# Performance work log

Hardware: AMD Instinct MI355X
Metric: run time of the kernel (lower is better)

## Reference

```python
import jax, jax.numpy as jnp
import numpy as np

WS = 8  # window size
NUM_HEAD = 8
DIM_HEAD = 64


def _rel_pos_index(ws):
    coords = np.stack(np.meshgrid(np.arange(ws), np.arange(ws), indexing='ij'))  # (2, ws, ws)
    cf = coords.reshape(2, -1)                       # (2, A)
    rel = cf[:, :, None] - cf[:, None, :]            # (2, A, A)
    rel = rel.transpose(1, 2, 0).astype(np.int32)    # (A, A, 2)
    rel[:, :, 0] += ws - 1
    rel[:, :, 1] += ws - 1
    rel[:, :, 0] *= 2 * ws - 1
    return jnp.asarray(rel.sum(-1))                  # (A, A) int32


def setup_inputs() -> dict:
    key = jax.random.key(0)
    k0, k1, k2 = jax.random.split(key, 3)
    B, Hh, dh, H, W = 4, NUM_HEAD, DIM_HEAD, 128, 128
    C = Hh * dh
    qkv = jax.random.normal(k0, (B, Hh, 3 * dh, H, W), dtype=jnp.float32)
    logit_scale = jnp.log(10.0) * jnp.ones((Hh, 1, 1), dtype=jnp.float32)
    rpb_table = 0.02 * jax.random.normal(k1, ((2 * WS - 1) * (2 * WS - 1), Hh), dtype=jnp.float32)
    proj_w = 0.02 * jax.random.normal(k2, (C, C), dtype=jnp.float32)
    proj_b = jnp.zeros((C,), dtype=jnp.float32)
    rel_index = _rel_pos_index(WS)
    return {"qkv": qkv, "logit_scale": logit_scale, "rpb_table": rpb_table,
            "proj_w": proj_w, "proj_b": proj_b, "rel_index": rel_index}


def reference(qkv, logit_scale, rpb_table, proj_w, proj_b, rel_index):
    B, Hh, C3, H, W = qkv.shape
    ws = WS
    dh = C3 // 3
    A = ws * ws
    nH, nW = H // ws, W // ws
    # window partition: (B, Hh, C3, H, W) -> (B*nH*nW, Hh, A, C3)
    x = qkv.reshape(B, Hh, C3, nH, ws, nW, ws)
    x = x.transpose(0, 3, 5, 1, 4, 6, 2).reshape(-1, Hh, A, C3)
    q, k, v = jnp.split(x, 3, axis=-1)
    # cosine attention: L2-normalize q, k (eps matches F.normalize)
    q = q / jnp.maximum(jnp.linalg.norm(q, axis=-1, keepdims=True), 1e-12)
    k = k / jnp.maximum(jnp.linalg.norm(k, axis=-1, keepdims=True), 1e-12)
    attn = jnp.einsum('whqd,whkd->whqk', q, k)
    scale = jnp.exp(jnp.minimum(logit_scale, jnp.log(100.0)))  # clamp max=log(1/0.01)
    attn = attn * scale[None]
    # relative position bias: (A,A,Hh) -> (1,Hh,A,A)
    bias = rpb_table[rel_index.reshape(-1)].reshape(A, A, Hh).transpose(2, 0, 1)
    attn = jax.nn.softmax(attn + bias[None], axis=-1)
    out = jnp.einsum('whqk,whkd->whqd', attn, v)  # (B*nH*nW, Hh, A, dh)
    # window unpartition -> (B, Hh*dh, H, W)
    out = out.reshape(B, nH, nW, Hh, ws, ws, dh)
    out = out.transpose(0, 3, 6, 1, 4, 2, 5).reshape(B, Hh * dh, H, W)
    # 1x1 conv projection
    out = jnp.einsum('oc,bchw->bohw', proj_w, out) + proj_b[None, :, None, None]
    return out
```

## Files before the change

### kernel.cpp

```cpp
#include <hip/hip_runtime.h>

typedef _Float16 f16;
typedef f16 f16x2 __attribute__((ext_vector_type(2)));
typedef f16 f16x4 __attribute__((ext_vector_type(4)));
typedef f16 f16x8 __attribute__((ext_vector_type(8)));
typedef float floatx4 __attribute__((ext_vector_type(4)));

#define LDS_AS(p) ((__attribute__((address_space(3))) unsigned int*)(p))
#define GLB_AS(p) ((const __attribute__((address_space(1))) unsigned int*)(p))

__device__ __forceinline__ void gload16(const void* g, void* l) {
  __builtin_amdgcn_global_load_lds(GLB_AS(g), LDS_AS(l), 16, 0, 0);
}

__global__ __launch_bounds__(256) void wconv_kernel(const float* __restrict__ w,
                                                    f16* __restrict__ wh) {
  const int i = (blockIdx.x * 256 + threadIdx.x) * 4;
  const float4 v = *(const float4*)(w + i);
  f16x4 o;
  o.x = (f16)v.x; o.y = (f16)v.y; o.z = (f16)v.z; o.w = (f16)v.w;
  *(f16x4*)(wh + i) = o;
}

__global__ __launch_bounds__(256) void attn_kernel(
    const float* __restrict__ qkv, const float* __restrict__ logit_scale,
    const float* __restrict__ rpb, const int* __restrict__ rel_index,
    f16* __restrict__ X) {
  __shared__ f16 qs[64 * 72];
  __shared__ f16 ks[64 * 72];
  __shared__ f16 vs[64 * 72];
  __shared__ f16 ps[64 * 72];
  __shared__ float partial[4][64];

  const int bid = blockIdx.x;
  const int h   = bid & 7;
  const int win = bid >> 3;
  const int wx  = win & 15;
  const int wy  = (win >> 4) & 15;
  const int b   = win >> 8;

  const int tid  = threadIdx.x;
  const int wave = tid >> 6;
  const int lane = tid & 63;

  {
    const int a  = lane;
    const int ty = a >> 3, tx = a & 7;
    const int poff = (wy * 8 + ty) * 128 + wx * 8 + tx;
    const size_t headbase = (size_t)((b * 8 + h) * 192) * 16384 + poff;
    const int cbase = (wave & 1) * 32;
    const int qk = (wave < 2) ? 0 : 64;
    const float* src = qkv + headbase + (size_t)(qk + cbase) * 16384;
    float vals[32];
    float ssq = 0.f;
#pragma unroll
    for (int i = 0; i < 32; i++) {
      float v = src[(size_t)i * 16384];
      vals[i] = v;
      ssq += v * v;
    }
    partial[wave][a] = ssq;

    const float* vsrc = qkv + headbase + (size_t)(128 + wave * 16) * 16384;
    float vv[16];
#pragma unroll
    for (int i = 0; i < 16; i++) vv[i] = vsrc[(size_t)i * 16384];

    __syncthreads();
    const float tot = partial[wave & 2][a] + partial[(wave & 2) | 1][a];
    const float rs = 1.0f / fmaxf(sqrtf(tot), 1e-12f);
    f16* dst = ((wave < 2) ? qs : ks) + a * 72 + cbase;
#pragma unroll
    for (int i = 0; i < 16; i++) {
      f16x2 pr;
      pr.x = (f16)(vals[2 * i] * rs);
      pr.y = (f16)(vals[2 * i + 1] * rs);
      *(f16x2*)(dst + 2 * i) = pr;
    }
#pragma unroll
    for (int i = 0; i < 16; i++) vs[(wave * 16 + i) * 72 + a] = (f16)vv[i];
  }
  __syncthreads();

  const int fr = lane & 15;
  const int g  = lane >> 4;
  const int m0 = wave * 16;
  const float scale = __expf(fminf(logit_scale[h], 4.60517019f));

  floatx4 acc[4];
  {
    const f16x8 a0 = *(const f16x8*)(qs + (m0 + fr) * 72 + g * 8);
    const f16x8 a1 = *(const f16x8*)(qs + (m0 + fr) * 72 + 32 + g * 8);
#pragma unroll
    for (int nt = 0; nt < 4; nt++) {
      const f16x8 b0 = *(const f16x8*)(ks + (nt * 16 + fr) * 72 + g * 8);
      const f16x8 b1 = *(const f16x8*)(ks + (nt * 16 + fr) * 72 + 32 + g * 8);
      floatx4 z = {0.f, 0.f, 0.f, 0.f};
      z = __builtin_amdgcn_mfma_f32_16x16x32_f16(a0, b0, z, 0, 0, 0);
      z = __builtin_amdgcn_mfma_f32_16x16x32_f16(a1, b1, z, 0, 0, 0);
      acc[nt] = z;
    }
  }

#pragma unroll
  for (int r = 0; r < 4; r++) {
    const int m = m0 + g * 4 + r;
    float v0[4];
    float mx = -1e30f;
#pragma unroll
    for (int nt = 0; nt < 4; nt++) {
      const int n = nt * 16 + fr;
      const float val = acc[nt][r] * scale + rpb[rel_index[m * 64 + n] * 8 + h];
      v0[nt] = val;
      mx = fmaxf(mx, val);
    }
    mx = fmaxf(mx, __shfl_xor(mx, 1));
    mx = fmaxf(mx, __shfl_xor(mx, 2));
    mx = fmaxf(mx, __shfl_xor(mx, 4));
    mx = fmaxf(mx, __shfl_xor(mx, 8));
    float s = 0.f;
#pragma unroll
    for (int nt = 0; nt < 4; nt++) {
      v0[nt] = __expf(v0[nt] - mx);
      s += v0[nt];
    }
    s += __shfl_xor(s, 1);
    s += __shfl_xor(s, 2);
    s += __shfl_xor(s, 4);
    s += __shfl_xor(s, 8);
    const float rinv = 1.0f / s;
#pragma unroll
    for (int nt = 0; nt < 4; nt++)
      ps[m * 72 + nt * 16 + fr] = (f16)(v0[nt] * rinv);
  }

  floatx4 oacc[4];
  {
    const f16x8 pa0 = *(const f16x8*)(ps + (m0 + fr) * 72 + g * 8);
    const f16x8 pa1 = *(const f16x8*)(ps + (m0 + fr) * 72 + 32 + g * 8);
#pragma unroll
    for (int dt = 0; dt < 4; dt++) {
      const f16x8 vb0 = *(const f16x8*)(vs + (dt * 16 + fr) * 72 + g * 8);
      const f16x8 vb1 = *(const f16x8*)(vs + (dt * 16 + fr) * 72 + 32 + g * 8);
      floatx4 z = {0.f, 0.f, 0.f, 0.f};
      z = __builtin_amdgcn_mfma_f32_16x16x32_f16(pa0, vb0, z, 0, 0, 0);
      z = __builtin_amdgcn_mfma_f32_16x16x32_f16(pa1, vb1, z, 0, 0, 0);
      oacc[dt] = z;
    }
  }

#pragma unroll
  for (int r = 0; r < 4; r++) {
    const int m = m0 + g * 4 + r;
    const int ty = m >> 3, tx = m & 7;
    const size_t npix = (size_t)(b * 128 + wy * 8 + ty) * 128 + wx * 8 + tx;
    f16* xp = X + npix * 512 + h * 64;
#pragma unroll
    for (int dt = 0; dt < 4; dt++) xp[dt * 16 + fr] = (f16)oacc[dt][r];
  }
}

__global__ __launch_bounds__(256) void proj_kernel(
    const f16* __restrict__ Wh, const f16* __restrict__ X,
    const float* __restrict__ bias, float* __restrict__ out) {
  __shared__ f16 As[128 * 32];
  __shared__ f16 Bs[128 * 32];

  const int tid  = threadIdx.x;
  const int lane = tid & 63;
  const int wave = tid >> 6;
  const int o0 = (blockIdx.x & 3) * 128;
  const int p0 = (blockIdx.x >> 2) * 128;

  const int fr = lane & 15, g = lane >> 4;
  const int wr = wave >> 1, wc = wave & 1;

  floatx4 acc[4][4] = {};

  const int r0 = tid >> 2;
  const int c0 = (tid & 3) * 8;
  const f16* gA0 = Wh + (size_t)(o0 + r0) * 512 + c0;
  const f16* gA1 = Wh + (size_t)(o0 + 64 + r0) * 512 + c0;
  const f16* gB0 = X + (size_t)(p0 + r0) * 512 + c0;
  const f16* gB1 = X + (size_t)(p0 + 64 + r0) * 512 + c0;
  f16* lA0 = As + tid * 8;
  f16* lA1 = As + (256 + tid) * 8;
  f16* lB0 = Bs + tid * 8;
  f16* lB1 = Bs + (256 + tid) * 8;

  for (int kc = 0; kc < 512; kc += 32) {
    gload16(gA0 + kc, lA0);
    gload16(gA1 + kc, lA1);
    gload16(gB0 + kc, lB0);
    gload16(gB1 + kc, lB1);
    __syncthreads();
    f16x8 af[4], bfr[4];
#pragma unroll
    for (int mt = 0; mt < 4; mt++)
      af[mt] = *(const f16x8*)(As + (wr * 64 + mt * 16 + fr) * 32 + g * 8);
#pragma unroll
    for (int nt = 0; nt < 4; nt++)
      bfr[nt] = *(const f16x8*)(Bs + (wc * 64 + nt * 16 + fr) * 32 + g * 8);
#pragma unroll
    for (int mt = 0; mt < 4; mt++)
#pragma unroll
      for (int nt = 0; nt < 4; nt++)
        acc[mt][nt] = __builtin_amdgcn_mfma_f32_16x16x32_f16(af[mt], bfr[nt],
                                                             acc[mt][nt], 0, 0, 0);
    __syncthreads();
  }

  const int bidx = p0 >> 14;
  const int rem0 = p0 & 16383;
#pragma unroll
  for (int mt = 0; mt < 4; mt++) {
#pragma unroll
    for (int r = 0; r < 4; r++) {
      const int o = o0 + wr * 64 + mt * 16 + g * 4 + r;
      const float bv = bias[o];
      float* op = out + ((size_t)(bidx * 512 + o) << 14) + rem0 + wc * 64;
#pragma unroll
      for (int nt = 0; nt < 4; nt++) op[nt * 16 + fr] = acc[mt][nt][r] + bv;
    }
  }
}

extern "C" void kernel_launch(void* const* d_in, const int* in_sizes, int n_in,
                              void* d_out, int out_size, void* d_ws, size_t ws_size,
                              hipStream_t stream) {
  const float* qkv         = (const float*)d_in[0];
  const float* logit_scale = (const float*)d_in[1];
  const float* rpb         = (const float*)d_in[2];
  const float* proj_w      = (const float*)d_in[3];
  const float* proj_b      = (const float*)d_in[4];
  const int*   rel_index   = (const int*)d_in[5];
  float* out = (float*)d_out;

  f16* Wh = (f16*)d_ws;
  f16* X  = (f16*)((char*)d_ws + (512 * 512 * 2));

  hipLaunchKernelGGL(wconv_kernel, dim3(256), dim3(256), 0, stream, proj_w, Wh);
  hipLaunchKernelGGL(attn_kernel, dim3(8192), dim3(256), 0, stream,
                     qkv, logit_scale, rpb, rel_index, X);
  hipLaunchKernelGGL(proj_kernel, dim3(2048), dim3(256), 0, stream,
                     Wh, X, proj_b, out);
}
```

Before: 653.3 us.

## Vectorize attention qkv loads and widen swizzled projection K tile

```diff
diff --git a/kernel.cpp b/kernel.cpp
--- a/kernel.cpp
+++ b/kernel.cpp
@@ -30,7 +30,6 @@
   __shared__ f16 ks[64 * 72];
   __shared__ f16 vs[64 * 72];
   __shared__ f16 ps[64 * 72];
-  __shared__ float partial[4][64];
 
   const int bid = blockIdx.x;
   const int h   = bid & 7;
@@ -44,41 +43,61 @@
   const int lane = tid & 63;
 
   {
-    const int a  = lane;
-    const int ty = a >> 3, tx = a & 7;
-    const int poff = (wy * 8 + ty) * 128 + wx * 8 + tx;
-    const size_t headbase = (size_t)((b * 8 + h) * 192) * 16384 + poff;
-    const int cbase = (wave & 1) * 32;
-    const int qk = (wave < 2) ? 0 : 64;
-    const float* src = qkv + headbase + (size_t)(qk + cbase) * 16384;
-    float vals[32];
+    const int c    = tid >> 2;
+    const int quad = tid & 3;
+    const int xh   = quad & 1;
+    const int tyb  = quad >> 1;
+    const size_t base = (size_t)((b * 8 + h) * 192) * 16384 +
+                        (size_t)(wy * 8) * 128 + wx * 8 + xh * 4;
+    const float* qp = qkv + base + (size_t)c * 16384;
+    const float* kp = qkv + base + (size_t)(64 + c) * 16384;
+    const float* vp = qkv + base + (size_t)(128 + c) * 16384;
+#pragma unroll
+    for (int j = 0; j < 4; j++) {
+      const int ty = 2 * j + tyb;
+      const int t0 = ty * 8 + xh * 4;
+      const float4 qv = *(const float4*)(qp + ty * 128);
+      const float4 kv = *(const float4*)(kp + ty * 128);
+      const float4 vv = *(const float4*)(vp + ty * 128);
+      qs[(t0 + 0) * 72 + c] = (f16)qv.x;
+      qs[(t0 + 1) * 72 + c] = (f16)qv.y;
+      qs[(t0 + 2) * 72 + c] = (f16)qv.z;
+      qs[(t0 + 3) * 72 + c] = (f16)qv.w;
+      ks[(t0 + 0) * 72 + c] = (f16)kv.x;
+      ks[(t0 + 1) * 72 + c] = (f16)kv.y;
+      ks[(t0 + 2) * 72 + c] = (f16)kv.z;
+      ks[(t0 + 3) * 72 + c] = (f16)kv.w;
+      vs[c * 72 + t0 + 0] = (f16)vv.x;
+      vs[c * 72 + t0 + 1] = (f16)vv.y;
+      vs[c * 72 + t0 + 2] = (f16)vv.z;
+      vs[c * 72 + t0 + 3] = (f16)vv.w;
+    }
+  }
+  __syncthreads();
+
+  {
+    const int token = (tid & 127) >> 1;
+    const int half  = tid & 1;
+    f16* rowp = ((tid < 128) ? qs : ks) + token * 72 + half * 32;
+    f16x8 d[4];
     float ssq = 0.f;
 #pragma unroll
-    for (int i = 0; i < 32; i++) {
-      float v = src[(size_t)i * 16384];
-      vals[i] = v;
-      ssq += v * v;
-    }
-    partial[wave][a] = ssq;
-
-    const float* vsrc = qkv + headbase + (size_t)(128 + wave * 16) * 16384;
-    float vv[16];
-#pragma unroll
-    for (int i = 0; i < 16; i++) vv[i] = vsrc[(size_t)i * 16384];
-
-    __syncthreads();
-    const float tot = partial[wave & 2][a] + partial[(wave & 2) | 1][a];
-    const float rs = 1.0f / fmaxf(sqrtf(tot), 1e-12f);
-    f16* dst = ((wave < 2) ? qs : ks) + a * 72 + cbase;
-#pragma unroll
-    for (int i = 0; i < 16; i++) {
-      f16x2 pr;
-      pr.x = (f16)(vals[2 * i] * rs);
-      pr.y = (f16)(vals[2 * i + 1] * rs);
-      *(f16x2*)(dst + 2 * i) = pr;
-    }
-#pragma unroll
-    for (int i = 0; i < 16; i++) vs[(wave * 16 + i) * 72 + a] = (f16)vv[i];
+    for (int i = 0; i < 4; i++) {
+      d[i] = *(const f16x8*)(rowp + i * 8);
+#pragma unroll
+      for (int e = 0; e < 8; e++) {
+        const float f = (float)d[i][e];
+        ssq += f * f;
+      }
+    }
+    ssq += __shfl_xor(ssq, 1);
+    const float rs = 1.0f / fmaxf(sqrtf(ssq), 1e-12f);
+#pragma unroll
+    for (int i = 0; i < 4; i++) {
+#pragma unroll
+      for (int e = 0; e < 8; e++) d[i][e] = (f16)((float)d[i][e] * rs);
+      *(f16x8*)(rowp + i * 8) = d[i];
+    }
   }
   __syncthreads();
 
@@ -163,8 +182,8 @@
 __global__ __launch_bounds__(256) void proj_kernel(
     const f16* __restrict__ Wh, const f16* __restrict__ X,
     const float* __restrict__ bias, float* __restrict__ out) {
-  __shared__ f16 As[128 * 32];
-  __shared__ f16 Bs[128 * 32];
+  __shared__ f16 As[128 * 64];
+  __shared__ f16 Bs[128 * 64];
 
   const int tid  = threadIdx.x;
   const int lane = tid & 63;
@@ -177,36 +196,44 @@
 
   floatx4 acc[4][4] = {};
 
-  const int r0 = tid >> 2;
-  const int c0 = (tid & 3) * 8;
-  const f16* gA0 = Wh + (size_t)(o0 + r0) * 512 + c0;
-  const f16* gA1 = Wh + (size_t)(o0 + 64 + r0) * 512 + c0;
-  const f16* gB0 = X + (size_t)(p0 + r0) * 512 + c0;
-  const f16* gB1 = X + (size_t)(p0 + 64 + r0) * 512 + c0;
-  f16* lA0 = As + tid * 8;
-  f16* lA1 = As + (256 + tid) * 8;
-  f16* lB0 = Bs + tid * 8;
-  f16* lB1 = Bs + (256 + tid) * 8;
-
-  for (int kc = 0; kc < 512; kc += 32) {
-    gload16(gA0 + kc, lA0);
-    gload16(gA1 + kc, lA1);
-    gload16(gB0 + kc, lB0);
-    gload16(gB1 + kc, lB1);
+  const f16* gA[4];
+  const f16* gB[4];
+#pragma unroll
+  for (int j = 0; j < 4; j++) {
+    const int slot = j * 256 + tid;
+    const int row  = slot >> 3;
+    const int c8   = (tid & 7) ^ (row & 7);
+    gA[j] = Wh + (size_t)(o0 + row) * 512 + c8 * 8;
+    gB[j] = X  + (size_t)(p0 + row) * 512 + c8 * 8;
+  }
+
+  for (int kc = 0; kc < 512; kc += 64) {
+#pragma unroll
+    for (int j = 0; j < 4; j++) {
+      gload16(gA[j] + kc, As + (j * 256 + tid) * 8);
+      gload16(gB[j] + kc, Bs + (j * 256 + tid) * 8);
+    }
     __syncthreads();
-    f16x8 af[4], bfr[4];
-#pragma unroll
-    for (int mt = 0; mt < 4; mt++)
-      af[mt] = *(const f16x8*)(As + (wr * 64 + mt * 16 + fr) * 32 + g * 8);
-#pragma unroll
-    for (int nt = 0; nt < 4; nt++)
-      bfr[nt] = *(const f16x8*)(Bs + (wc * 64 + nt * 16 + fr) * 32 + g * 8);
-#pragma unroll
-    for (int mt = 0; mt < 4; mt++)
-#pragma unroll
-      for (int nt = 0; nt < 4; nt++)
-        acc[mt][nt] = __builtin_amdgcn_mfma_f32_16x16x32_f16(af[mt], bfr[nt],
-                                                             acc[mt][nt], 0, 0, 0);
+#pragma unroll
+    for (int kk = 0; kk < 2; kk++) {
+      f16x8 af[4], bfr[4];
+#pragma unroll
+      for (int mt = 0; mt < 4; mt++) {
+        const int row = wr * 64 + mt * 16 + fr;
+        af[mt] = *(const f16x8*)(As + row * 64 + (((kk * 4 + g) ^ (row & 7)) * 8));
+      }
+#pragma unroll
+      for (int nt = 0; nt < 4; nt++) {
+        const int row = wc * 64 + nt * 16 + fr;
+        bfr[nt] = *(const f16x8*)(Bs + row * 64 + (((kk * 4 + g) ^ (row & 7)) * 8));
+      }
+#pragma unroll
+      for (int mt = 0; mt < 4; mt++)
+#pragma unroll
+        for (int nt = 0; nt < 4; nt++)
+          acc[mt][nt] = __builtin_amdgcn_mfma_f32_16x16x32_f16(af[mt], bfr[nt],
+                                                               acc[mt][nt], 0, 0, 0);
+    }
     __syncthreads();
   }
 
```

Measured after the change: 643.6 us. Within noise of the previous version (-1.5%).
